# Kernel tuning notes

Hardware: AMD Instinct MI355X
Metric: run time of the kernel (lower is better)

Reference implementation:

```python
import jax, jax.numpy as jnp
import numpy as np

VOCAB = 32000
MAXLEN = 512
E = 768
H = 12
D = E // H  # 64
L = 6
F = int(E * 8 / 3)  # 2048
THETA = 10000.0
EPS = 1.1920929e-07  # torch.finfo(float32).eps, RMSNorm default


def _rms_norm(x, w):
    var = jnp.mean(x * x, axis=-1, keepdims=True)
    return x * jax.lax.rsqrt(var + EPS) * w


def _rope(x, cos, sin):
    # x: [B,H,C,D]; cos/sin: [C,D/2] (interleaved even/odd convention)
    xe = x[..., 0::2]
    xo = x[..., 1::2]
    re = xe * cos - xo * sin
    ro = xe * sin + xo * cos
    out = jnp.stack([re, ro], axis=-1)  # [B,H,C,D/2,2]
    return out.reshape(x.shape)


def setup_inputs() -> dict:
    key = jax.random.key(0)
    ks = jax.random.split(key, 13)
    s = 0.02
    ids = jax.random.randint(ks[0], (8, MAXLEN), 0, VOCAB)
    embed = jax.random.normal(ks[1], (VOCAB, E), jnp.float32) * s
    norm1_w = jnp.ones((L, E), jnp.float32)
    wq = jax.random.normal(ks[2], (L, E, H * D), jnp.float32) * s
    wk = jax.random.normal(ks[3], (L, E, H * D), jnp.float32) * s
    wv = jax.random.normal(ks[4], (L, E, H * D), jnp.float32) * s
    wo = jax.random.normal(ks[5], (L, H * D, E), jnp.float32) * s
    norm2_w = jnp.ones((L, E), jnp.float32)
    w_gate = jax.random.normal(ks[6], (L, E, F), jnp.float32) * s
    w_val = jax.random.normal(ks[7], (L, E, F), jnp.float32) * s
    w_out = jax.random.normal(ks[8], (L, F, E), jnp.float32) * s
    normf_w = jnp.ones((E,), jnp.float32)
    unembed = jax.random.normal(ks[9], (E, VOCAB), jnp.float32) * s
    return {"ids": ids, "embed": embed, "norm1_w": norm1_w, "wq": wq,
            "wk": wk, "wv": wv, "wo": wo, "norm2_w": norm2_w,
            "w_gate": w_gate, "w_val": w_val, "w_out": w_out,
            "normf_w": normf_w, "unembed": unembed}


def reference(ids, embed, norm1_w, wq, wk, wv, wo, norm2_w,
              w_gate, w_val, w_out, normf_w, unembed):
    B, C = ids.shape
    # RoPE caches [C, D/2]
    half_ids = jnp.arange(D // 2, dtype=jnp.float32)
    inv_freq = 1.0 / (THETA ** (2.0 * half_ids / D))
    angles = jnp.arange(C, dtype=jnp.float32)[:, None] * inv_freq[None, :]
    cos, sin = jnp.cos(angles), jnp.sin(angles)
    causal = jnp.tril(jnp.ones((C, C), bool))

    x = embed[ids]  # [B,C,E]
    for l in range(L):
        h = _rms_norm(x, norm1_w[l])
        q = (h @ wq[l]).reshape(B, C, H, D).transpose(0, 2, 1, 3)
        k = (h @ wk[l]).reshape(B, C, H, D).transpose(0, 2, 1, 3)
        v = (h @ wv[l]).reshape(B, C, H, D).transpose(0, 2, 1, 3)
        q = _rope(q, cos, sin)
        k = _rope(k, cos, sin)
        scores = jnp.einsum('bhqd,bhkd->bhqk', q, k) / jnp.sqrt(jnp.float32(D))
        scores = jnp.where(causal, scores, -jnp.inf)
        w = jax.nn.softmax(scores, axis=-1)
        attn = jnp.einsum('bhqk,bhkd->bhqd', w, v)
        attn = attn.transpose(0, 2, 1, 3).reshape(B, C, H * D)
        x = x + attn @ wo[l]
        h2 = _rms_norm(x, norm2_w[l])
        gated = jax.nn.silu(h2 @ w_gate[l]) * (h2 @ w_val[l])
        x = x + gated @ w_out[l]
    x = _rms_norm(x, normf_w)
    return x @ unembed  # [B,C,VOCAB]
```

## Files before the change

### kernel.cpp

```cpp
#include <hip/hip_runtime.h>
#include <hip/hip_bf16.h>
#include <stdint.h>

typedef __hip_bfloat16 bf16;
typedef unsigned short ushort_t;
typedef __attribute__((ext_vector_type(8))) short bf16x8;
typedef __attribute__((ext_vector_type(4))) float f32x4;

#define EPSV 1.1920929e-07f

__device__ __forceinline__ float bfu2f(uint32_t u) {
  union { uint32_t i; float f; } t; t.i = u << 16; return t.f;
}
__device__ __forceinline__ ushort_t f2bfu(float f) {
  bf16 h = __float2bfloat16(f);
  return *reinterpret_cast<ushort_t*>(&h);
}

#define BAR() __builtin_amdgcn_s_barrier()
#define SCHEDB() __builtin_amdgcn_sched_barrier(0)
#define WAIT_LGKM0() { asm volatile("s_waitcnt lgkmcnt(0)" ::: "memory"); SCHEDB(); }
#define WAIT_VM4() asm volatile("s_waitcnt vmcnt(4)" ::: "memory")
#define WAIT_VM0() asm volatile("s_waitcnt vmcnt(0)" ::: "memory")

__global__ void rope_table_kernel(float* __restrict__ cosT, float* __restrict__ sinT) {
  int i = blockIdx.x * 256 + threadIdx.x;
  if (i >= 512 * 32) return;
  int c = i >> 5, dp = i & 31;
  float inv = powf(10000.0f, -(2.0f * dp) / 64.0f);
  float a = (float)c * inv;
  cosT[i] = cosf(a);
  sinT[i] = sinf(a);
}

__global__ void embed_kernel(const int* __restrict__ ids, const float* __restrict__ emb,
                             float* __restrict__ x) {
  int t = blockIdx.x;
  int id = ids[t];
  const float4* s = (const float4*)(emb + (size_t)id * 768);
  float4* d = (float4*)(x + (size_t)t * 768);
  d[threadIdx.x] = s[threadIdx.x];
}

__global__ __launch_bounds__(256) void rmsnorm_kernel(const float* __restrict__ x,
                                                      const float* __restrict__ wgt,
                                                      bf16* __restrict__ out) {
  const int row = blockIdx.x;
  const int tid = threadIdx.x;
  const float* xr = x + (size_t)row * 768;
  float v0 = xr[tid], v1 = xr[tid + 256], v2 = xr[tid + 512];
  float s = v0 * v0 + v1 * v1 + v2 * v2;
#pragma unroll
  for (int d = 1; d < 64; d <<= 1) s += __shfl_xor(s, d);
  __shared__ float red[4];
  if ((tid & 63) == 0) red[tid >> 6] = s;
  __syncthreads();
  s = red[0] + red[1] + red[2] + red[3];
  float rs = rsqrtf(s * (1.0f / 768.0f) + EPSV);
  bf16* orow = out + (size_t)row * 768;
  orow[tid]       = __float2bfloat16(v0 * rs * wgt[tid]);
  orow[tid + 256] = __float2bfloat16(v1 * rs * wgt[tid + 256]);
  orow[tid + 512] = __float2bfloat16(v2 * rs * wgt[tid + 512]);
}

__global__ __launch_bounds__(256) void rope_qk_kernel(bf16* __restrict__ qkv,
                                                      const float* __restrict__ cosT,
                                                      const float* __restrict__ sinT) {
  int idx = blockIdx.x * 256 + threadIdx.x;
  int t = idx / 384, rem = idx - t * 384;
  int h = rem >> 5, dp = rem & 31;
  int c = t & 511;
  float cs = cosT[c * 32 + dp], sn = sinT[c * 32 + dp];
  bf16* qp = qkv + (size_t)t * 2304 + h * 64 + dp * 2;
  uint32_t uq = *(const uint32_t*)qp;
  float xe = bfu2f(uq & 0xffffu), xo = bfu2f(uq >> 16);
  float re = (xe * cs - xo * sn) * 0.125f;
  float ro = (xe * sn + xo * cs) * 0.125f;
  *(uint32_t*)qp = (uint32_t)f2bfu(re) | ((uint32_t)f2bfu(ro) << 16);
  bf16* kp = qp + 768;
  uint32_t uk = *(const uint32_t*)kp;
  xe = bfu2f(uk & 0xffffu); xo = bfu2f(uk >> 16);
  *(uint32_t*)kp = (uint32_t)f2bfu(xe * cs - xo * sn) | ((uint32_t)f2bfu(xe * sn + xo * cs) << 16);
}

__global__ __launch_bounds__(256) void transpose_all_kernel(
    const float* __restrict__ wq, const float* __restrict__ wk,
    const float* __restrict__ wv, const float* __restrict__ wo,
    const float* __restrict__ wg, const float* __restrict__ wvl,
    const float* __restrict__ wout, const float* __restrict__ unemb,
    bf16* __restrict__ wqkvT, bf16* __restrict__ woT,
    bf16* __restrict__ wgvT, bf16* __restrict__ woutT,
    bf16* __restrict__ unembT) {
  int id = blockIdx.x;
  const float* src; bf16* dst; int K, N, tile;
  bool gvmode = false; int w2 = 0;
  if (id < 13824) {
    int m = id / 576; tile = id % 576;
    int l = m >> 2, w3 = m & 3;
    K = 768; N = 768;
    const float* s0 = (w3 == 0) ? wq : (w3 == 1) ? wk : (w3 == 2) ? wv : wo;
    src = s0 + (size_t)l * 768 * 768;
    dst = (w3 < 3) ? wqkvT + (size_t)l * 2304 * 768 + (size_t)w3 * 768 * 768
                   : woT + (size_t)l * 768 * 768;
  } else if (id < 32256) {
    int id2 = id - 13824; int m = id2 / 1536; tile = id2 % 1536;
    int l = m >> 1; w2 = m & 1;
    K = 768; N = 2048; gvmode = true;
    src = (w2 ? wvl : wg) + (size_t)l * 768 * 2048;
    dst = wgvT + (size_t)l * 4096 * 768;
  } else if (id < 41472) {
    int id2 = id - 32256; int l = id2 / 1536; tile = id2 % 1536;
    K = 2048; N = 768;
    src = wout + (size_t)l * 2048 * 768;
    dst = woutT + (size_t)l * 768 * 2048;
  } else {
    tile = id - 41472;
    K = 768; N = 32000;
    src = unemb; dst = unembT;
  }
  int ntn = N >> 5;
  int nt = (tile % ntn) << 5, kt = (tile / ntn) << 5;
  __shared__ float tl[32][33];
  int tx = threadIdx.x & 31, ty = threadIdx.x >> 5;
#pragma unroll
  for (int i = 0; i < 4; ++i)
    tl[ty + i * 8][tx] = src[(size_t)(kt + ty + i * 8) * N + nt + tx];
  __syncthreads();
#pragma unroll
  for (int i = 0; i < 4; ++i) {
    int n = nt + ty + i * 8;
    size_t nrow = gvmode ? (size_t)((n >> 7) * 256 + w2 * 128 + (n & 127)) : (size_t)n;
    dst[nrow * K + kt + tx] = __float2bfloat16(tl[tx][ty + i * 8]);
  }
}

template <int MODE>
__global__ __launch_bounds__(256) void gemm_bt(const bf16* __restrict__ A,
                                               const bf16* __restrict__ BT,
                                               void* __restrict__ C,
                                               int M, int N, int K) {
  __shared__ __align__(16) bf16 As[128 * 32];
  __shared__ __align__(16) bf16 Bs[128 * 32];
  const int tid = threadIdx.x;
  const int lane = tid & 63, w = tid >> 6;
  const int g = lane >> 4, lc = lane & 15;
  const int bm = blockIdx.y * 128, bn = blockIdx.x * 128;
  const int wm = (w >> 1) * 64, wn = (w & 1) * 64;

  f32x4 acc[4][4];
#pragma unroll
  for (int i = 0; i < 4; ++i)
#pragma unroll
    for (int j = 0; j < 4; ++j) acc[i][j] = (f32x4){0.f, 0.f, 0.f, 0.f};

  for (int k0 = 0; k0 < K; k0 += 32) {
    __syncthreads();
#pragma unroll
    for (int j = 0; j < 2; ++j) {
      int c = (w * 2 + j) * 64 + lane;
      int row = c >> 2, part = c & 3;
      const bf16* srcA = A + (size_t)(bm + row) * K + k0 + part * 8;
      const bf16* srcB = BT + (size_t)(bn + row) * K + k0 + part * 8;
      __builtin_amdgcn_global_load_lds((const __attribute__((address_space(1))) void*)srcA,
                                       (__attribute__((address_space(3))) void*)(As + (w * 2 + j) * 512),
                                       16, 0, 0);
      __builtin_amdgcn_global_load_lds((const __attribute__((address_space(1))) void*)srcB,
                                       (__attribute__((address_space(3))) void*)(Bs + (w * 2 + j) * 512),
                                       16, 0, 0);
    }
    __syncthreads();
    bf16x8 af[4], bfr[4];
#pragma unroll
    for (int mi = 0; mi < 4; ++mi)
      af[mi] = *(const bf16x8*)(As + (wm + mi * 16 + lc) * 32 + g * 8);
#pragma unroll
    for (int ni = 0; ni < 4; ++ni)
      bfr[ni] = *(const bf16x8*)(Bs + (wn + ni * 16 + lc) * 32 + g * 8);
#pragma unroll
    for (int mi = 0; mi < 4; ++mi)
#pragma unroll
      for (int ni = 0; ni < 4; ++ni)
        acc[mi][ni] = __builtin_amdgcn_mfma_f32_16x16x32_bf16(af[mi], bfr[ni], acc[mi][ni], 0, 0, 0);
  }

#pragma unroll
  for (int mi = 0; mi < 4; ++mi)
#pragma unroll
    for (int ni = 0; ni < 4; ++ni)
#pragma unroll
      for (int r = 0; r < 4; ++r) {
        size_t row = (size_t)bm + wm + mi * 16 + g * 4 + r;
        size_t col = (size_t)bn + wn + ni * 16 + lc;
        float v = acc[mi][ni][r];
        if (MODE == 0)      ((bf16*)C)[row * N + col] = __float2bfloat16(v);
        else if (MODE == 1) ((float*)C)[row * N + col] = v;
        else                ((float*)C)[row * N + col] += v;
      }
}

template <int MODE>
__global__ __launch_bounds__(512, 2) void gemm256(const bf16* __restrict__ A,
                                                  const bf16* __restrict__ BT,
                                                  void* __restrict__ C,
                                                  int M, int N, int K) {
  __shared__ __align__(16) bf16 lds[2][4][256 * 32];

  const int tid = threadIdx.x;
  const int lane = tid & 63, w = tid >> 6;
  const int wr = w >> 2, wc = w & 3;
  const int g = lane >> 4, lc = lane & 15;

  const int nwg = gridDim.x;
  const int q = nwg >> 3;
  const int wg = ((int)blockIdx.x & 7) * q + ((int)blockIdx.x >> 3);
  const int nby = M >> 8;
  const int bx = wg / nby, by = wg % nby;
  const int bm = by << 8, bn = bx << 8;

  const bf16* Ap = A + (size_t)bm * K;
  const bf16* Bp = BT + (size_t)bn * K;

  const int soff = (lc * 64) + ((((lane >> 4) ^ ((lane >> 1) & 3)) << 4));

  auto stage_half = [&](int buf, int slab, const bf16* Base, int kcol) {
#pragma unroll
    for (int j = 0; j < 2; ++j) {
      int half_id = w * 2 + j;
      int row = half_id * 16 + (lane >> 2);
      int s_log = (lane & 3) ^ ((lane >> 3) & 3);
      const bf16* src = Base + (size_t)row * K + kcol + s_log * 8;
      bf16* dst = &lds[buf][slab][half_id * 512];
      __builtin_amdgcn_global_load_lds((const __attribute__((address_space(1))) void*)src,
                                       (__attribute__((address_space(3))) void*)dst,
                                       16, 0, 0);
    }
  };

  f32x4 acc[8][4];
#pragma unroll
  for (int i = 0; i < 8; ++i)
#pragma unroll
    for (int j = 0; j < 4; ++j) acc[i][j] = (f32x4){0.f, 0.f, 0.f, 0.f};

  const int NT = K >> 6;

  stage_half(0, 0, Ap, 0);
  stage_half(0, 1, Bp, 0);
  stage_half(0, 2, Ap, 32);
  stage_half(0, 3, Bp, 32);

  bf16x8 aF[4], bF[4];

  auto ds_A = [&](int buf, int kk, int mh) {
#pragma unroll
    for (int i = 0; i < 4; ++i) {
      int byte = (wr * 128 + mh * 64 + i * 16) * 64 + soff;
      aF[i] = *(const bf16x8*)((const char*)&lds[buf][kk * 2][0] + byte);
    }
  };
  auto ds_B = [&](int buf, int kk) {
#pragma unroll
    for (int nf = 0; nf < 4; ++nf) {
      int rb = (MODE == 3) ? ((nf < 2) ? (wc * 32 + nf * 16) : (128 + wc * 32 + (nf - 2) * 16))
                           : (wc * 64 + nf * 16);
      int byte = rb * 64 + soff;
      bF[nf] = *(const bf16x8*)((const char*)&lds[buf][kk * 2 + 1][0] + byte);
    }
  };
  auto mfma16 = [&](int mh) {
    __builtin_amdgcn_s_setprio(1);
#pragma unroll
    for (int i = 0; i < 4; ++i)
#pragma unroll
      for (int nf = 0; nf < 4; ++nf)
        acc[mh * 4 + i][nf] =
            __builtin_amdgcn_mfma_f32_16x16x32_bf16(aF[i], bF[nf], acc[mh * 4 + i][nf], 0, 0, 0);
    __builtin_amdgcn_s_setprio(0);
  };

  for (int t = 0; t < NT; ++t) {
    const int buf = t & 1;
    const bool pf = (t + 1) < NT;
    const int knext = (t + 1) << 6;

    WAIT_VM4();
    BAR(); SCHEDB();
    if (pf) stage_half(buf ^ 1, 0, Ap, knext);
    ds_A(buf, 0, 0);
    ds_B(buf, 0);
    BAR();
    WAIT_LGKM0();
    mfma16(0);

    if (pf) stage_half(buf ^ 1, 1, Bp, knext);
    ds_A(buf, 0, 1);
    BAR();
    WAIT_LGKM0();
    mfma16(1);

    if (pf) { WAIT_VM4(); } else { WAIT_VM0(); }
    BAR(); SCHEDB();
    if (pf) stage_half(buf ^ 1, 2, Ap, knext + 32);
    ds_A(buf, 1, 0);
    ds_B(buf, 1);
    BAR();
    WAIT_LGKM0();
    mfma16(0);

    if (pf) stage_half(buf ^ 1, 3, Bp, knext + 32);
    ds_A(buf, 1, 1);
    BAR();
    WAIT_LGKM0();
    mfma16(1);
  }

  if (MODE == 3) {
    bf16* act = (bf16*)C;
#pragma unroll
    for (int mf = 0; mf < 8; ++mf)
#pragma unroll
      for (int nf = 0; nf < 2; ++nf)
#pragma unroll
        for (int r = 0; r < 4; ++r) {
          size_t row = (size_t)bm + wr * 128 + mf * 16 + g * 4 + r;
          size_t col = (size_t)(bn >> 1) + wc * 32 + nf * 16 + lc;
          float gg = acc[mf][nf][r];
          float vv = acc[mf][nf + 2][r];
          float sg = gg / (1.0f + __expf(-gg));
          act[row * 2048 + col] = __float2bfloat16(sg * vv);
        }
  } else {
#pragma unroll
    for (int mf = 0; mf < 8; ++mf)
#pragma unroll
      for (int nf = 0; nf < 4; ++nf)
#pragma unroll
        for (int r = 0; r < 4; ++r) {
          size_t row = (size_t)bm + wr * 128 + mf * 16 + g * 4 + r;
          size_t col = (size_t)bn + wc * 64 + nf * 16 + lc;
          float v = acc[mf][nf][r];
          if (MODE == 0) ((bf16*)C)[row * N + col] = __float2bfloat16(v);
          else           ((float*)C)[row * N + col] = v;
        }
  }
}

__global__ __launch_bounds__(256) void attn_kernel(const bf16* __restrict__ qkv,
                                                   bf16* __restrict__ out) {
  const int qt = blockIdx.x;
  const int h  = blockIdx.y;
  const int b  = blockIdx.z;
  const int tid = threadIdx.x;
  const int lane = tid & 63, w = tid >> 6;
  const int g = lane >> 4, lc = lane & 15;

  __shared__ __align__(16) bf16 Ks[64][72];
  __shared__ __align__(16) bf16 Vt[64][72];
  __shared__ __align__(16) bf16 Pl[4][32][72];

  bf16x8 qa[2][2];
#pragma unroll
  for (int mi = 0; mi < 2; ++mi)
#pragma unroll
    for (int ks = 0; ks < 2; ++ks) {
      size_t t = (size_t)b * 512 + qt * 128 + w * 32 + mi * 16 + lc;
      qa[mi][ks] = *(const bf16x8*)(qkv + t * 2304 + h * 64 + ks * 32 + g * 8);
    }

  float m_r[2][4], l_r[2][4];
  f32x4 acc_o[2][4];
#pragma unroll
  for (int mi = 0; mi < 2; ++mi)
#pragma unroll
    for (int r = 0; r < 4; ++r) { m_r[mi][r] = -1e30f; l_r[mi][r] = 0.f; }
#pragma unroll
  for (int mi = 0; mi < 2; ++mi)
#pragma unroll
    for (int ni = 0; ni < 4; ++ni) acc_o[mi][ni] = (f32x4){0.f, 0.f, 0.f, 0.f};

  const int nkt = 2 * qt + 2;
  for (int kt = 0; kt < nkt; ++kt) {
    __syncthreads();
    for (int i = 0; i < 8; ++i) {
      int pi = i * 256 + tid;
      int r = pi >> 5, dp = pi & 31;
      size_t t = (size_t)b * 512 + kt * 64 + r;
      uint32_t u = *(const uint32_t*)(qkv + t * 2304 + 768 + h * 64 + dp * 2);
      *(uint32_t*)&Ks[r][dp * 2] = u;
      uint32_t uv = *(const uint32_t*)(qkv + t * 2304 + 1536 + h * 64 + dp * 2);
      *(ushort_t*)&Vt[dp * 2][r]     = (ushort_t)(uv & 0xffffu);
      *(ushort_t*)&Vt[dp * 2 + 1][r] = (ushort_t)(uv >> 16);
    }
    __syncthreads();

    f32x4 sacc[2][4];
#pragma unroll
    for (int mi = 0; mi < 2; ++mi)
#pragma unroll
      for (int ni = 0; ni < 4; ++ni) sacc[mi][ni] = (f32x4){0.f, 0.f, 0.f, 0.f};
#pragma unroll
    for (int ni = 0; ni < 4; ++ni) {
      bf16x8 kb0 = *(const bf16x8*)&Ks[ni * 16 + lc][g * 8];
      bf16x8 kb1 = *(const bf16x8*)&Ks[ni * 16 + lc][32 + g * 8];
#pragma unroll
      for (int mi = 0; mi < 2; ++mi) {
        sacc[mi][ni] = __builtin_amdgcn_mfma_f32_16x16x32_bf16(qa[mi][0], kb0, sacc[mi][ni], 0, 0, 0);
        sacc[mi][ni] = __builtin_amdgcn_mfma_f32_16x16x32_bf16(qa[mi][1], kb1, sacc[mi][ni], 0, 0, 0);
      }
    }
    if (kt >= 2 * qt) {
#pragma unroll
      for (int mi = 0; mi < 2; ++mi)
#pragma unroll
        for (int ni = 0; ni < 4; ++ni)
#pragma unroll
          for (int r = 0; r < 4; ++r) {
            int ql = w * 32 + mi * 16 + g * 4 + r;
            int kl = ni * 16 + lc;
            if (kt * 64 + kl > qt * 128 + ql) sacc[mi][ni][r] = -1e30f;
          }
    }
#pragma unroll
    for (int mi = 0; mi < 2; ++mi) {
      float mx[4], sm[4], mn[4], sc[4];
#pragma unroll
      for (int r = 0; r < 4; ++r)
        mx[r] = fmaxf(fmaxf(sacc[mi][0][r], sacc[mi][1][r]), fmaxf(sacc[mi][2][r], sacc[mi][3][r]));
#pragma unroll
      for (int d = 1; d < 16; d <<= 1)
#pragma unroll
        for (int r = 0; r < 4; ++r) mx[r] = fmaxf(mx[r], __shfl_xor(mx[r], d));
#pragma unroll
      for (int r = 0; r < 4; ++r) {
        mn[r] = fmaxf(m_r[mi][r], mx[r]);
        sc[r] = __expf(m_r[mi][r] - mn[r]);
        sm[r] = 0.f;
      }
#pragma unroll
      for (int ni = 0; ni < 4; ++ni)
#pragma unroll
        for (int r = 0; r < 4; ++r) {
          float p = __expf(sacc[mi][ni][r] - mn[r]);
          sacc[mi][ni][r] = p;
          sm[r] += p;
        }
#pragma unroll
      for (int d = 1; d < 16; d <<= 1)
#pragma unroll
        for (int r = 0; r < 4; ++r) sm[r] += __shfl_xor(sm[r], d);
#pragma unroll
      for (int r = 0; r < 4; ++r) {
        l_r[mi][r] = l_r[mi][r] * sc[r] + sm[r];
        m_r[mi][r] = mn[r];
      }
#pragma unroll
      for (int ni = 0; ni < 4; ++ni)
#pragma unroll
        for (int r = 0; r < 4; ++r) acc_o[mi][ni][r] *= sc[r];
#pragma unroll
      for (int ni = 0; ni < 4; ++ni)
#pragma unroll
        for (int r = 0; r < 4; ++r)
          *(ushort_t*)&Pl[w][mi * 16 + g * 4 + r][ni * 16 + lc] = f2bfu(sacc[mi][ni][r]);
    }
    __syncthreads();
#pragma unroll
    for (int ks = 0; ks < 2; ++ks) {
      bf16x8 pa[2];
#pragma unroll
      for (int mi = 0; mi < 2; ++mi)
        pa[mi] = *(const bf16x8*)&Pl[w][mi * 16 + lc][ks * 32 + g * 8];
#pragma unroll
      for (int ni = 0; ni < 4; ++ni) {
        bf16x8 vb = *(const bf16x8*)&Vt[ni * 16 + lc][ks * 32 + g * 8];
#pragma unroll
        for (int mi = 0; mi < 2; ++mi)
          acc_o[mi][ni] = __builtin_amdgcn_mfma_f32_16x16x32_bf16(pa[mi], vb, acc_o[mi][ni], 0, 0, 0);
      }
    }
  }
#pragma unroll
  for (int mi = 0; mi < 2; ++mi) {
    float inv[4];
#pragma unroll
    for (int r = 0; r < 4; ++r) inv[r] = 1.0f / l_r[mi][r];
#pragma unroll
    for (int ni = 0; ni < 4; ++ni)
#pragma unroll
      for (int r = 0; r < 4; ++r) {
        size_t t = (size_t)b * 512 + qt * 128 + w * 32 + mi * 16 + g * 4 + r;
        int d = ni * 16 + lc;
        out[t * 768 + h * 64 + d] = __float2bfloat16(acc_o[mi][ni][r] * inv[r]);
      }
  }
}

extern "C" void kernel_launch(void* const* d_in, const int* in_sizes, int n_in,
                              void* d_out, int out_size, void* d_ws, size_t ws_size,
                              hipStream_t stream) {
  const int*   ids    = (const int*)d_in[0];
  const float* embedW = (const float*)d_in[1];
  const float* norm1w = (const float*)d_in[2];
  const float* wq     = (const float*)d_in[3];
  const float* wk     = (const float*)d_in[4];
  const float* wv     = (const float*)d_in[5];
  const float* wo     = (const float*)d_in[6];
  const float* norm2w = (const float*)d_in[7];
  const float* wgate  = (const float*)d_in[8];
  const float* wval   = (const float*)d_in[9];
  const float* wout   = (const float*)d_in[10];
  const float* normfw = (const float*)d_in[11];
  const float* unemb  = (const float*)d_in[12];

  char* arena = (char*)d_out;
  size_t off = 0;
  auto alloc = [&](size_t bytes) -> char* {
    char* p = arena + off;
    off += (bytes + 255) & ~(size_t)255;
    return p;
  };
  float* x       = (float*)alloc(4096ull * 768 * 4);
  bf16*  h       = (bf16*)alloc(4096ull * 768 * 2);
  bf16*  qkv     = (bf16*)alloc(4096ull * 2304 * 2);
  bf16*  attnout = (bf16*)alloc(4096ull * 768 * 2);
  bf16*  act     = (bf16*)alloc(4096ull * 2048 * 2);
  float* cosT    = (float*)alloc(512 * 32 * 4);
  float* sinT    = (float*)alloc(512 * 32 * 4);
  bf16*  wqkvT   = (bf16*)alloc(6ull * 2304 * 768 * 2);
  bf16*  woT     = (bf16*)alloc(6ull * 768 * 768 * 2);
  bf16*  wgvT    = (bf16*)alloc(6ull * 4096 * 768 * 2);
  bf16*  woutT   = (bf16*)alloc(6ull * 768 * 2048 * 2);

  bf16* unembT = (bf16*)d_ws;
  bf16* hf     = (bf16*)((char*)d_ws + 32000ull * 768 * 2);

  rope_table_kernel<<<64, 256, 0, stream>>>(cosT, sinT);
  embed_kernel<<<4096, 192, 0, stream>>>(ids, embedW, x);
  transpose_all_kernel<<<65472, 256, 0, stream>>>(wq, wk, wv, wo, wgate, wval, wout, unemb,
                                                  wqkvT, woT, wgvT, woutT, unembT);

  for (int l = 0; l < 6; ++l) {
    rmsnorm_kernel<<<4096, 256, 0, stream>>>(x, norm1w + (size_t)l * 768, h);
    gemm256<0><<<16 * 9, 512, 0, stream>>>(h, wqkvT + (size_t)l * 2304 * 768, qkv, 4096, 2304, 768);
    rope_qk_kernel<<<6144, 256, 0, stream>>>(qkv, cosT, sinT);
    attn_kernel<<<dim3(4, 12, 8), 256, 0, stream>>>(qkv, attnout);
    gemm_bt<2><<<dim3(6, 32), 256, 0, stream>>>(attnout, woT + (size_t)l * 768 * 768, x, 4096, 768, 768);
    rmsnorm_kernel<<<4096, 256, 0, stream>>>(x, norm2w + (size_t)l * 768, h);
    gemm256<3><<<16 * 16, 512, 0, stream>>>(h, wgvT + (size_t)l * 4096 * 768, act, 4096, 4096, 768);
    gemm_bt<2><<<dim3(6, 32), 256, 0, stream>>>(act, woutT + (size_t)l * 768 * 2048, x, 4096, 768, 2048);
  }

  rmsnorm_kernel<<<4096, 256, 0, stream>>>(x, normfw, hf);
  gemm256<1><<<16 * 125, 512, 0, stream>>>(hf, unembT, (float*)d_out, 4096, 32000, 768);
}
```

Baseline: 1.644 ms.

## Fuse RoPE into QKV GEMM epilogue and stage K via direct global-to-LDS loads

The separate RoPE kernel is removed. RoPE and the 1/sqrt(D) query scale are now applied in a new gemm256 epilogue mode, which pairs even and odd columns with a lane shuffle. The attention kernel loads K tiles straight into a swizzled LDS layout using global_load_lds and loads V with 16-byte vector reads before transposing it. A __syncthreads before the P·V step is replaced by a local lgkmcnt wait. Together these remove a full read and write pass over Q and K per layer and reduce load instructions in attention. The risk is correctness of the async LDS load ordering and of the wait-only sync, since each wave only reads its own Pl slice.

```diff
diff --git a/kernel.cpp b/kernel.cpp
--- a/kernel.cpp
+++ b/kernel.cpp
@@ -61,26 +61,6 @@
   orow[tid]       = __float2bfloat16(v0 * rs * wgt[tid]);
   orow[tid + 256] = __float2bfloat16(v1 * rs * wgt[tid + 256]);
   orow[tid + 512] = __float2bfloat16(v2 * rs * wgt[tid + 512]);
-}
-
-__global__ __launch_bounds__(256) void rope_qk_kernel(bf16* __restrict__ qkv,
-                                                      const float* __restrict__ cosT,
-                                                      const float* __restrict__ sinT) {
-  int idx = blockIdx.x * 256 + threadIdx.x;
-  int t = idx / 384, rem = idx - t * 384;
-  int h = rem >> 5, dp = rem & 31;
-  int c = t & 511;
-  float cs = cosT[c * 32 + dp], sn = sinT[c * 32 + dp];
-  bf16* qp = qkv + (size_t)t * 2304 + h * 64 + dp * 2;
-  uint32_t uq = *(const uint32_t*)qp;
-  float xe = bfu2f(uq & 0xffffu), xo = bfu2f(uq >> 16);
-  float re = (xe * cs - xo * sn) * 0.125f;
-  float ro = (xe * sn + xo * cs) * 0.125f;
-  *(uint32_t*)qp = (uint32_t)f2bfu(re) | ((uint32_t)f2bfu(ro) << 16);
-  bf16* kp = qp + 768;
-  uint32_t uk = *(const uint32_t*)kp;
-  xe = bfu2f(uk & 0xffffu); xo = bfu2f(uk >> 16);
-  *(uint32_t*)kp = (uint32_t)f2bfu(xe * cs - xo * sn) | ((uint32_t)f2bfu(xe * sn + xo * cs) << 16);
 }
 
 __global__ __launch_bounds__(256) void transpose_all_kernel(
@@ -202,7 +182,9 @@
 __global__ __launch_bounds__(512, 2) void gemm256(const bf16* __restrict__ A,
                                                   const bf16* __restrict__ BT,
                                                   void* __restrict__ C,
-                                                  int M, int N, int K) {
+                                                  int M, int N, int K,
+                                                  const float* __restrict__ cosT,
+                                                  const float* __restrict__ sinT) {
   __shared__ __align__(16) bf16 lds[2][4][256 * 32];
 
   const int tid = threadIdx.x;
@@ -329,6 +311,27 @@
           float sg = gg / (1.0f + __expf(-gg));
           act[row * 2048 + col] = __float2bfloat16(sg * vv);
         }
+  } else if (MODE == 4) {
+#pragma unroll
+    for (int mf = 0; mf < 8; ++mf)
+#pragma unroll
+      for (int nf = 0; nf < 4; ++nf)
+#pragma unroll
+        for (int r = 0; r < 4; ++r) {
+          int row = bm + wr * 128 + mf * 16 + g * 4 + r;
+          int col = bn + wc * 64 + nf * 16 + lc;
+          float v = acc[mf][nf][r];
+          float p = __shfl_xor(v, 1);
+          float outv = v;
+          if (col < 1536) {
+            int cpos = row & 511;
+            int dp = (col & 63) >> 1;
+            float cs = cosT[cpos * 32 + dp], sn = sinT[cpos * 32 + dp];
+            float o = (col & 1) ? (p * sn + v * cs) : (v * cs - p * sn);
+            outv = (col < 768) ? o * 0.125f : o;
+          }
+          ((bf16*)C)[(size_t)row * N + col] = __float2bfloat16(outv);
+        }
   } else {
 #pragma unroll
     for (int mf = 0; mf < 8; ++mf)
@@ -354,7 +357,7 @@
   const int lane = tid & 63, w = tid >> 6;
   const int g = lane >> 4, lc = lane & 15;
 
-  __shared__ __align__(16) bf16 Ks[64][72];
+  __shared__ __align__(16) bf16 Ks[64 * 64];
   __shared__ __align__(16) bf16 Vt[64][72];
   __shared__ __align__(16) bf16 Pl[4][32][72];
 
@@ -381,15 +384,25 @@
   const int nkt = 2 * qt + 2;
   for (int kt = 0; kt < nkt; ++kt) {
     __syncthreads();
-    for (int i = 0; i < 8; ++i) {
-      int pi = i * 256 + tid;
-      int r = pi >> 5, dp = pi & 31;
-      size_t t = (size_t)b * 512 + kt * 64 + r;
-      uint32_t u = *(const uint32_t*)(qkv + t * 2304 + 768 + h * 64 + dp * 2);
-      *(uint32_t*)&Ks[r][dp * 2] = u;
-      uint32_t uv = *(const uint32_t*)(qkv + t * 2304 + 1536 + h * 64 + dp * 2);
-      *(ushort_t*)&Vt[dp * 2][r]     = (ushort_t)(uv & 0xffffu);
-      *(ushort_t*)&Vt[dp * 2 + 1][r] = (ushort_t)(uv >> 16);
+#pragma unroll
+    for (int j = 0; j < 2; ++j) {
+      int c = j * 256 + tid;
+      int r = c >> 3;
+      int s_log = (c & 7) ^ (r & 7);
+      const bf16* src = qkv + ((size_t)b * 512 + kt * 64 + r) * 2304 + 768 + h * 64 + s_log * 8;
+      bf16* dst = Ks + (j * 2048 + w * 512);
+      __builtin_amdgcn_global_load_lds((const __attribute__((address_space(1))) void*)src,
+                                       (__attribute__((address_space(3))) void*)dst,
+                                       16, 0, 0);
+    }
+#pragma unroll
+    for (int j = 0; j < 2; ++j) {
+      int u = j * 256 + tid;
+      int r = u >> 3, d0 = (u & 7) * 8;
+      bf16x8 vv = *(const bf16x8*)(qkv + ((size_t)b * 512 + kt * 64 + r) * 2304 + 1536 + h * 64 + d0);
+#pragma unroll
+      for (int e = 0; e < 8; ++e)
+        *(ushort_t*)&Vt[d0 + e][r] = (ushort_t)vv[e];
     }
     __syncthreads();
 
@@ -400,8 +413,10 @@
       for (int ni = 0; ni < 4; ++ni) sacc[mi][ni] = (f32x4){0.f, 0.f, 0.f, 0.f};
 #pragma unroll
     for (int ni = 0; ni < 4; ++ni) {
-      bf16x8 kb0 = *(const bf16x8*)&Ks[ni * 16 + lc][g * 8];
-      bf16x8 kb1 = *(const bf16x8*)&Ks[ni * 16 + lc][32 + g * 8];
+      int kr = ni * 16 + lc;
+      const char* kb = (const char*)Ks + kr * 128;
+      bf16x8 kb0 = *(const bf16x8*)(kb + ((g) ^ (kr & 7)) * 16);
+      bf16x8 kb1 = *(const bf16x8*)(kb + ((4 + g) ^ (kr & 7)) * 16);
 #pragma unroll
       for (int mi = 0; mi < 2; ++mi) {
         sacc[mi][ni] = __builtin_amdgcn_mfma_f32_16x16x32_bf16(qa[mi][0], kb0, sacc[mi][ni], 0, 0, 0);
@@ -463,7 +478,7 @@
         for (int r = 0; r < 4; ++r)
           *(ushort_t*)&Pl[w][mi * 16 + g * 4 + r][ni * 16 + lc] = f2bfu(sacc[mi][ni][r]);
     }
-    __syncthreads();
+    WAIT_LGKM0();
 #pragma unroll
     for (int ks = 0; ks < 2; ++ks) {
       bf16x8 pa[2];
@@ -541,15 +556,17 @@
 
   for (int l = 0; l < 6; ++l) {
     rmsnorm_kernel<<<4096, 256, 0, stream>>>(x, norm1w + (size_t)l * 768, h);
-    gemm256<0><<<16 * 9, 512, 0, stream>>>(h, wqkvT + (size_t)l * 2304 * 768, qkv, 4096, 2304, 768);
-    rope_qk_kernel<<<6144, 256, 0, stream>>>(qkv, cosT, sinT);
+    gemm256<4><<<16 * 9, 512, 0, stream>>>(h, wqkvT + (size_t)l * 2304 * 768, qkv,
+                                           4096, 2304, 768, cosT, sinT);
     attn_kernel<<<dim3(4, 12, 8), 256, 0, stream>>>(qkv, attnout);
     gemm_bt<2><<<dim3(6, 32), 256, 0, stream>>>(attnout, woT + (size_t)l * 768 * 768, x, 4096, 768, 768);
     rmsnorm_kernel<<<4096, 256, 0, stream>>>(x, norm2w + (size_t)l * 768, h);
-    gemm256<3><<<16 * 16, 512, 0, stream>>>(h, wgvT + (size_t)l * 4096 * 768, act, 4096, 4096, 768);
+    gemm256<3><<<16 * 16, 512, 0, stream>>>(h, wgvT + (size_t)l * 4096 * 768, act,
+                                            4096, 4096, 768, nullptr, nullptr);
     gemm_bt<2><<<dim3(6, 32), 256, 0, stream>>>(act, woutT + (size_t)l * 768 * 2048, x, 4096, 768, 2048);
   }
 
   rmsnorm_kernel<<<4096, 256, 0, stream>>>(x, normfw, hf);
-  gemm256<1><<<16 * 125, 512, 0, stream>>>(hf, unembT, (float*)d_out, 4096, 32000, 768);
-}
+  gemm256<1><<<16 * 125, 512, 0, stream>>>(hf, unembT, (float*)d_out, 4096, 32000, 768,
+                                           nullptr, nullptr);
+}
```

After: 1.736 ms. 5.6% more time.
